# Kernel optimization log

Measured on AMD Instinct MI355X. Metric: run time of the kernel, lower is better.

The kernel has to match this reference:

```python
import jax, jax.numpy as jnp
import numpy as np


def setup_inputs() -> dict:
    key = jax.random.key(0)
    kq, kk, kv = jax.random.split(key, 3)
    shape = (2, 12, 4096, 64)  # [B, H, S, d]
    Q = jax.random.normal(kq, shape, dtype=jnp.float32)
    K = jax.random.normal(kk, shape, dtype=jnp.float32)
    V = jax.random.normal(kv, shape, dtype=jnp.float32)
    return {"Q": Q, "K": K, "V": V}


def reference(Q, K, V):
    d_k = K.shape[-1]
    scale = 1.0 / jnp.sqrt(jnp.asarray(d_k, dtype=Q.dtype))
    # [B,H,S,S] attention scores
    scores = jnp.einsum('bhqd,bhkd->bhqk', Q, K) * scale
    attn = jax.nn.softmax(scores, axis=-1)
    out = jnp.einsum('bhqk,bhkd->bhqd', attn, V)
    return out
```

## Files before the change

kernel.cpp:

```cpp
#include <hip/hip_runtime.h>


constexpr int Sseq = 4096;
constexpr int Dh   = 64;
constexpr int BM   = 128;
constexpr int BN   = 64;
constexpr int NT   = Sseq / BN;
constexpr float SHIFT = 10.0f;
constexpr float CINIT = -SHIFT + 0.002815047f;

typedef short bf16x8 __attribute__((ext_vector_type(8)));
typedef float f32x4  __attribute__((ext_vector_type(4)));

__device__ __forceinline__ unsigned short f2bf(float x) {
    union { float f; unsigned int u; } v; v.f = x;
    unsigned int r = v.u + 0x7fffu + ((v.u >> 16) & 1u);
    return (unsigned short)(r >> 16);
}

#if __has_builtin(__builtin_amdgcn_exp2f)
#define EXP2(x) __builtin_amdgcn_exp2f(x)
#else
#define EXP2(x) exp2f(x)
#endif

__device__ __forceinline__ int swz(int row, int blk8) {
    return row * 8 + (blk8 ^ (row & 7));
}

__device__ __forceinline__ void gld16(const void* g, void* l) {
    __builtin_amdgcn_global_load_lds(
        (const __attribute__((address_space(1))) void*)g,
        (__attribute__((address_space(3))) void*)l, 16, 0, 0);
}

union AFrag { unsigned int w[4]; bf16x8 b; };

__device__ __forceinline__ void s_phase(const unsigned short* __restrict__ sK,
                                        const bf16x8 (&qf)[2][2], f32x4 cinit,
                                        int lo, int quad, AFrag (&afW)[2][2]) {
    #pragma unroll
    for (int t = 0; t < 4; ++t) {
        const bf16x8 k0 = *reinterpret_cast<const bf16x8*>(&sK[swz(16 * t + lo, quad) * 8]);
        const bf16x8 k1 = *reinterpret_cast<const bf16x8*>(&sK[swz(16 * t + lo, 4 + quad) * 8]);
        #pragma unroll
        for (int u = 0; u < 2; ++u) {
            f32x4 s = __builtin_amdgcn_mfma_f32_16x16x32_bf16(k1, qf[u][1], cinit, 0, 0, 0);
            s = __builtin_amdgcn_mfma_f32_16x16x32_bf16(k0, qf[u][0], s, 0, 0, 0);
            union { float f; unsigned int v; } e0, e1, e2, e3;
            e0.f = EXP2(s[0]); e1.f = EXP2(s[1]);
            e2.f = EXP2(s[2]); e3.f = EXP2(s[3]);
            afW[u][t >> 1].w[2 * (t & 1) + 0] = __builtin_amdgcn_perm(e1.v, e0.v, 0x07060302u);
            afW[u][t >> 1].w[2 * (t & 1) + 1] = __builtin_amdgcn_perm(e3.v, e2.v, 0x07060302u);
        }
    }
}

__device__ __forceinline__ void pv_phase(const unsigned short* __restrict__ sVt,
                                         const AFrag (&afR)[2][2], bf16x8 onesb,
                                         int lo, int quad,
                                         f32x4 (&accv)[2][4], f32x4 (&acc5)[2]) {
    #pragma unroll
    for (int c = 0; c < 2; ++c) {
        #pragma unroll
        for (int u = 0; u < 2; ++u)
            acc5[u] = __builtin_amdgcn_mfma_f32_16x16x32_bf16(afR[u][c].b, onesb, acc5[u], 0, 0, 0);
        #pragma unroll
        for (int t2 = 0; t2 < 4; ++t2) {
            const bf16x8 vf = *reinterpret_cast<const bf16x8*>(&sVt[swz(16 * t2 + lo, 4 * c + quad) * 8]);
            #pragma unroll
            for (int u = 0; u < 2; ++u)
                accv[u][t2] = __builtin_amdgcn_mfma_f32_16x16x32_bf16(afR[u][c].b, vf, accv[u][t2], 0, 0, 0);
        }
    }
}

__global__ __launch_bounds__(256)
void preconv_kernel(const float* __restrict__ K, const float* __restrict__ V,
                    unsigned short* __restrict__ ws)
{
    __shared__ unsigned short tile[8192];
    unsigned short* tK = tile;
    unsigned short* tV = tile + 4096;

    const int kb = blockIdx.x, bh = blockIdx.y, tid = threadIdx.x;
    const float4* k4 = reinterpret_cast<const float4*>(K + ((size_t)bh * Sseq + kb * BN) * Dh);
    const float4* v4 = reinterpret_cast<const float4*>(V + ((size_t)bh * Sseq + kb * BN) * Dh);
    unsigned short* kimg = ws + (size_t)(bh * NT + kb) * 8192;

    float4 kv[4], vv[4];
    #pragma unroll
    for (int it = 0; it < 4; ++it) kv[it] = k4[it * 256 + tid];
    #pragma unroll
    for (int it = 0; it < 4; ++it) vv[it] = v4[it * 256 + tid];

    #pragma unroll
    for (int it = 0; it < 4; ++it) {
        const int f  = it * 256 + tid;
        const int r  = f >> 4;
        const int c4 = (f & 15) * 4;
        const int pr = (r & 32) | ((r & 4) << 2) | ((r & 24) >> 1) | (r & 3);
        unsigned int lo32 = (unsigned int)f2bf(kv[it].x) | ((unsigned int)f2bf(kv[it].y) << 16);
        unsigned int hi32 = (unsigned int)f2bf(kv[it].z) | ((unsigned int)f2bf(kv[it].w) << 16);
        *reinterpret_cast<uint2*>(&tK[swz(pr, c4 >> 3) * 8 + (c4 & 7)]) = make_uint2(lo32, hi32);
        tV[swz(c4 + 0, r >> 3) * 8 + (r & 7)] = f2bf(vv[it].x);
        tV[swz(c4 + 1, r >> 3) * 8 + (r & 7)] = f2bf(vv[it].y);
        tV[swz(c4 + 2, r >> 3) * 8 + (r & 7)] = f2bf(vv[it].z);
        tV[swz(c4 + 3, r >> 3) * 8 + (r & 7)] = f2bf(vv[it].w);
    }
    __syncthreads();

    const uint4* src = reinterpret_cast<const uint4*>(tile);
    uint4* dst = reinterpret_cast<uint4*>(kimg);
    #pragma unroll
    for (int i = 0; i < 4; ++i)
        dst[i * 256 + tid] = src[i * 256 + tid];
}

__global__ __launch_bounds__(256, 3)
void fattn_kernel(const float* __restrict__ Q, const unsigned short* __restrict__ ws,
                  float* __restrict__ O)
{
    __shared__ unsigned short sKV[3][8192];

    const int tid  = threadIdx.x;
    const int wave = tid >> 6;
    const int lane = tid & 63;
    const int lo   = lane & 15;
    const int quad = lane >> 4;

    const int qblk = blockIdx.x;
    const int bh   = blockIdx.y;

    const float* gQ = Q + (size_t)bh * Sseq * Dh;
    float*       gO = O + (size_t)bh * Sseq * Dh;

    const float qscale = 0.18033688011112042f;
    bf16x8 qf[2][2];
    #pragma unroll
    for (int u = 0; u < 2; ++u) {
        const int qrow = qblk * BM + wave * 32 + u * 16 + lo;
        const float* qp = gQ + (size_t)qrow * Dh + quad * 8;
        #pragma unroll
        for (int c = 0; c < 2; ++c) {
            float4 a = *reinterpret_cast<const float4*>(qp + c * 32);
            float4 b = *reinterpret_cast<const float4*>(qp + c * 32 + 4);
            qf[u][c][0] = (short)f2bf(a.x * qscale);
            qf[u][c][1] = (short)f2bf(a.y * qscale);
            qf[u][c][2] = (short)f2bf(a.z * qscale);
            qf[u][c][3] = (short)f2bf(a.w * qscale);
            qf[u][c][4] = (short)f2bf(b.x * qscale);
            qf[u][c][5] = (short)f2bf(b.y * qscale);
            qf[u][c][6] = (short)f2bf(b.z * qscale);
            qf[u][c][7] = (short)f2bf(b.w * qscale);
        }
    }

    bf16x8 onesb = (bf16x8)0;
    if (lo == 0) {
        #pragma unroll
        for (int j = 0; j < 8; ++j) onesb[j] = (short)0x3F80;
    }

    const f32x4 cinit = f32x4{CINIT, CINIT, CINIT, CINIT};

    f32x4 accv[2][4];
    f32x4 acc5[2];
    #pragma unroll
    for (int u = 0; u < 2; ++u) {
        acc5[u] = f32x4{0.f, 0.f, 0.f, 0.f};
        #pragma unroll
        for (int t = 0; t < 4; ++t) accv[u][t] = f32x4{0.f, 0.f, 0.f, 0.f};
    }

    AFrag afA[2][2], afB[2][2];

    const char* img = (const char*)(ws + (size_t)bh * NT * 8192);
    const int ubase = wave * 1024;
    const int goff  = ubase + lane * 16;

    auto dma = [&](int tile, int bufidx) {
        const char* nimg = img + (size_t)tile * 16384;
        char* dst = (char*)sKV[bufidx];
        gld16(nimg + goff,          dst + ubase);
        gld16(nimg + 4096  + goff,  dst + 4096  + ubase);
        gld16(nimg + 8192  + goff,  dst + 8192  + ubase);
        gld16(nimg + 12288 + goff,  dst + 12288 + ubase);
    };

    dma(0, 0);
    __syncthreads();
    dma(1, 1);
    s_phase(sKV[0], qf, cinit, lo, quad, afA);
    __syncthreads();
    dma(2, 2);

    int ibS = 1, ibP = 0;
    auto half = [&](int i, AFrag (&afW)[2][2], const AFrag (&afR)[2][2]) {
        const unsigned short* sK  = sKV[ibS];
        const unsigned short* sVt = sKV[ibP] + 4096;
        __builtin_amdgcn_s_setprio(1);
        s_phase(sK, qf, cinit, lo, quad, afW);
        pv_phase(sVt, afR, onesb, lo, quad, accv, acc5);
        __builtin_amdgcn_s_setprio(0);
        __syncthreads();
        if (i + 2 < NT) dma(i + 2, ibP);
        ibP = ibS;
        ibS = (ibS == 2) ? 0 : ibS + 1;
    };

    int i = 1;
    #pragma unroll 1
    for (int p = 0; p < 31; ++p) {
        half(i, afB, afA); ++i;
        half(i, afA, afB); ++i;
    }
    half(63, afB, afA);
    pv_phase(sKV[ibP] + 4096, afB, onesb, lo, quad, accv, acc5);

    #pragma unroll
    for (int u = 0; u < 2; ++u) {
        const int qbase = qblk * BM + wave * 32 + u * 16 + quad * 4;
        #pragma unroll
        for (int r = 0; r < 4; ++r) {
            const float ls  = __shfl(acc5[u][r], (lane & 48));
            const float inv = 1.0f / ls;
            float* op = gO + (size_t)(qbase + r) * Dh;
            #pragma unroll
            for (int t2 = 0; t2 < 4; ++t2)
                op[t2 * 16 + lo] = accv[u][t2][r] * inv;
        }
    }
}

constexpr int LD = 72;
__global__ __launch_bounds__(256, 2)
void fattn_fallback(const float* __restrict__ Q, const float* __restrict__ K,
                    const float* __restrict__ V, float* __restrict__ O)
{
    __shared__ unsigned short sK [BN * LD];
    __shared__ unsigned short sVt[Dh * LD];
    __shared__ unsigned short sP [4 * 16 * LD];

    const int tid  = threadIdx.x;
    const int wave = tid >> 6;
    const int lane = tid & 63;
    const int lo   = lane & 15;
    const int quad = lane >> 4;
    const int qblk = blockIdx.x;
    const int bh   = blockIdx.y;

    const float* gQ = Q + (size_t)bh * Sseq * Dh;
    const float* gK = K + (size_t)bh * Sseq * Dh;
    const float* gV = V + (size_t)bh * Sseq * Dh;
    float*       gO = O + (size_t)bh * Sseq * Dh;

    const float qscale = 0.18033688011112042f;
    bf16x8 qf[2];
    {
        const int qrow = qblk * 64 + wave * 16 + lo;
        const float* qp = gQ + (size_t)qrow * Dh + quad * 8;
        #pragma unroll
        for (int c = 0; c < 2; ++c) {
            float4 a = *reinterpret_cast<const float4*>(qp + c * 32);
            float4 b = *reinterpret_cast<const float4*>(qp + c * 32 + 4);
            qf[c][0] = (short)f2bf(a.x * qscale); qf[c][1] = (short)f2bf(a.y * qscale);
            qf[c][2] = (short)f2bf(a.z * qscale); qf[c][3] = (short)f2bf(a.w * qscale);
            qf[c][4] = (short)f2bf(b.x * qscale); qf[c][5] = (short)f2bf(b.y * qscale);
            qf[c][6] = (short)f2bf(b.z * qscale); qf[c][7] = (short)f2bf(b.w * qscale);
        }
    }

    float m_prev[4] = {-1e30f, -1e30f, -1e30f, -1e30f};
    float lsum[4]   = {0.f, 0.f, 0.f, 0.f};
    f32x4 accv[4];
    #pragma unroll
    for (int t = 0; t < 4; ++t) accv[t] = f32x4{0.f, 0.f, 0.f, 0.f};
    unsigned short* sPw = &sP[wave * 16 * LD];

    for (int kb = 0; kb < Sseq / BN; ++kb) {
        const float4* k4 = reinterpret_cast<const float4*>(gK + (size_t)kb * BN * Dh);
        const float4* v4 = reinterpret_cast<const float4*>(gV + (size_t)kb * BN * Dh);
        #pragma unroll
        for (int it = 0; it < 4; ++it) {
            const int f   = it * 256 + tid;
            const int row = f >> 4;
            const int c4  = (f & 15) * 4;
            float4 kv = k4[f];
            unsigned int lo32 = (unsigned int)f2bf(kv.x) | ((unsigned int)f2bf(kv.y) << 16);
            unsigned int hi32 = (unsigned int)f2bf(kv.z) | ((unsigned int)f2bf(kv.w) << 16);
            *reinterpret_cast<uint2*>(&sK[row * LD + c4]) = make_uint2(lo32, hi32);
            float4 vv = v4[f];
            sVt[(c4 + 0) * LD + row] = f2bf(vv.x);
            sVt[(c4 + 1) * LD + row] = f2bf(vv.y);
            sVt[(c4 + 2) * LD + row] = f2bf(vv.z);
            sVt[(c4 + 3) * LD + row] = f2bf(vv.w);
        }
        __syncthreads();

        float sc[4][4];
        #pragma unroll
        for (int t = 0; t < 4; ++t) {
            const bf16x8 k0 = *reinterpret_cast<const bf16x8*>(&sK[(t * 16 + lo) * LD + 0  + quad * 8]);
            const bf16x8 k1 = *reinterpret_cast<const bf16x8*>(&sK[(t * 16 + lo) * LD + 32 + quad * 8]);
            f32x4 s = f32x4{0.f, 0.f, 0.f, 0.f};
            s = __builtin_amdgcn_mfma_f32_16x16x32_bf16(qf[0], k0, s, 0, 0, 0);
            s = __builtin_amdgcn_mfma_f32_16x16x32_bf16(qf[1], k1, s, 0, 0, 0);
            sc[t][0] = s[0]; sc[t][1] = s[1]; sc[t][2] = s[2]; sc[t][3] = s[3];
        }

        float bm[4];
        #pragma unroll
        for (int r = 0; r < 4; ++r)
            bm[r] = fmaxf(fmaxf(sc[0][r], sc[1][r]), fmaxf(sc[2][r], sc[3][r]));
        #pragma unroll
        for (int m = 1; m <= 8; m <<= 1) {
            #pragma unroll
            for (int r = 0; r < 4; ++r) bm[r] = fmaxf(bm[r], __shfl_xor(bm[r], m));
        }
        float m_new[4], alpha[4];
        #pragma unroll
        for (int r = 0; r < 4; ++r) {
            m_new[r] = fmaxf(m_prev[r], bm[r]);
            alpha[r] = exp2f(m_prev[r] - m_new[r]);
            m_prev[r] = m_new[r];
        }
        float ps[4][4];
        float rs[4] = {0.f, 0.f, 0.f, 0.f};
        #pragma unroll
        for (int t = 0; t < 4; ++t) {
            #pragma unroll
            for (int r = 0; r < 4; ++r) { ps[t][r] = exp2f(sc[t][r] - m_new[r]); rs[r] += ps[t][r]; }
        }
        #pragma unroll
        for (int m = 1; m <= 8; m <<= 1) {
            #pragma unroll
            for (int r = 0; r < 4; ++r) rs[r] += __shfl_xor(rs[r], m);
        }
        #pragma unroll
        for (int r = 0; r < 4; ++r) lsum[r] = lsum[r] * alpha[r] + rs[r];
        #pragma unroll
        for (int t = 0; t < 4; ++t) {
            #pragma unroll
            for (int r = 0; r < 4; ++r) accv[t][r] *= alpha[r];
        }
        #pragma unroll
        for (int t = 0; t < 4; ++t) {
            #pragma unroll
            for (int r = 0; r < 4; ++r)
                sPw[(quad * 4 + r) * LD + t * 16 + lo] = f2bf(ps[t][r]);
        }
        #pragma unroll
        for (int c = 0; c < 2; ++c) {
            const bf16x8 af = *reinterpret_cast<const bf16x8*>(&sPw[lo * LD + c * 32 + quad * 8]);
            #pragma unroll
            for (int t2 = 0; t2 < 4; ++t2) {
                const bf16x8 vf = *reinterpret_cast<const bf16x8*>(&sVt[(t2 * 16 + lo) * LD + c * 32 + quad * 8]);
                accv[t2] = __builtin_amdgcn_mfma_f32_16x16x32_bf16(af, vf, accv[t2], 0, 0, 0);
            }
        }
        __syncthreads();
    }

    const int qbase = qblk * 64 + wave * 16 + quad * 4;
    #pragma unroll
    for (int r = 0; r < 4; ++r) {
        const float inv = 1.0f / lsum[r];
        float* op = gO + (size_t)(qbase + r) * Dh;
        #pragma unroll
        for (int t2 = 0; t2 < 4; ++t2)
            op[t2 * 16 + lo] = accv[t2][r] * inv;
    }
}

extern "C" void kernel_launch(void* const* d_in, const int* in_sizes, int n_in,
                              void* d_out, int out_size, void* d_ws, size_t ws_size,
                              hipStream_t stream) {
    const float* Q = (const float*)d_in[0];
    const float* K = (const float*)d_in[1];
    const float* V = (const float*)d_in[2];
    float* O = (float*)d_out;
    const int BH = in_sizes[0] / (Sseq * Dh);
    const size_t ws_needed = (size_t)BH * NT * 16384;
    if (ws_size >= ws_needed) {
        preconv_kernel<<<dim3(NT, BH), 256, 0, stream>>>(K, V, (unsigned short*)d_ws);
        fattn_kernel<<<dim3(Sseq / BM, BH), 256, 0, stream>>>(Q, (const unsigned short*)d_ws, O);
    } else {
        fattn_fallback<<<dim3(Sseq / 64, BH), 256, 0, stream>>>(Q, K, V, O);
    }
}
```

Measured before the change: 203.6 us.

## Load V fragments directly from global into registers, shrink LDS to double-buffered K

V tiles are no longer staged through LDS. Each wave now reads its pre-swizzled bf16 V fragments straight from the global workspace into registers at the start of each step, while only K keeps a two-slot LDS double buffer. This cuts LDS use from three 16KB buffers to two 8KB ones, which could raise occupancy, and removes the V LDS reads. In exchange, every wave issues redundant global loads for V with less latency hiding and more register pressure.

```diff
diff --git a/kernel.cpp b/kernel.cpp
--- a/kernel.cpp
+++ b/kernel.cpp
@@ -56,10 +56,19 @@
     }
 }
 
-__device__ __forceinline__ void pv_phase(const unsigned short* __restrict__ sVt,
-                                         const AFrag (&afR)[2][2], bf16x8 onesb,
-                                         int lo, int quad,
-                                         f32x4 (&accv)[2][4], f32x4 (&acc5)[2]) {
+__device__ __forceinline__ void pv_load(const char* __restrict__ vimg,
+                                        const unsigned int (&voff)[2][4],
+                                        bf16x8 (&vfr)[2][4]) {
+    #pragma unroll
+    for (int c = 0; c < 2; ++c)
+        #pragma unroll
+        for (int t2 = 0; t2 < 4; ++t2)
+            vfr[c][t2] = *reinterpret_cast<const bf16x8*>(vimg + voff[c][t2]);
+}
+
+__device__ __forceinline__ void pv_mfma(const bf16x8 (&vfr)[2][4],
+                                        const AFrag (&afR)[2][2], bf16x8 onesb,
+                                        f32x4 (&accv)[2][4], f32x4 (&acc5)[2]) {
     #pragma unroll
     for (int c = 0; c < 2; ++c) {
         #pragma unroll
@@ -67,10 +76,9 @@
             acc5[u] = __builtin_amdgcn_mfma_f32_16x16x32_bf16(afR[u][c].b, onesb, acc5[u], 0, 0, 0);
         #pragma unroll
         for (int t2 = 0; t2 < 4; ++t2) {
-            const bf16x8 vf = *reinterpret_cast<const bf16x8*>(&sVt[swz(16 * t2 + lo, 4 * c + quad) * 8]);
             #pragma unroll
             for (int u = 0; u < 2; ++u)
-                accv[u][t2] = __builtin_amdgcn_mfma_f32_16x16x32_bf16(afR[u][c].b, vf, accv[u][t2], 0, 0, 0);
+                accv[u][t2] = __builtin_amdgcn_mfma_f32_16x16x32_bf16(afR[u][c].b, vfr[c][t2], accv[u][t2], 0, 0, 0);
         }
     }
 }
@@ -121,7 +129,7 @@
 void fattn_kernel(const float* __restrict__ Q, const unsigned short* __restrict__ ws,
                   float* __restrict__ O)
 {
-    __shared__ unsigned short sKV[3][8192];
+    __shared__ unsigned short sKk[2][4096];
 
     const int tid  = threadIdx.x;
     const int wave = tid >> 6;
@@ -164,6 +172,13 @@
 
     const f32x4 cinit = f32x4{CINIT, CINIT, CINIT, CINIT};
 
+    unsigned int voff[2][4];
+    #pragma unroll
+    for (int c = 0; c < 2; ++c)
+        #pragma unroll
+        for (int t2 = 0; t2 < 4; ++t2)
+            voff[c][t2] = (unsigned int)(swz(16 * t2 + lo, 4 * c + quad) * 16);
+
     f32x4 accv[2][4];
     f32x4 acc5[2];
     #pragma unroll
@@ -179,34 +194,28 @@
     const int ubase = wave * 1024;
     const int goff  = ubase + lane * 16;
 
-    auto dma = [&](int tile, int bufidx) {
+    auto dmaK = [&](int tile, int bufidx) {
         const char* nimg = img + (size_t)tile * 16384;
-        char* dst = (char*)sKV[bufidx];
-        gld16(nimg + goff,          dst + ubase);
-        gld16(nimg + 4096  + goff,  dst + 4096  + ubase);
-        gld16(nimg + 8192  + goff,  dst + 8192  + ubase);
-        gld16(nimg + 12288 + goff,  dst + 12288 + ubase);
+        char* dst = (char*)sKk[bufidx];
+        gld16(nimg + goff,         dst + ubase);
+        gld16(nimg + 4096 + goff,  dst + 4096 + ubase);
     };
 
-    dma(0, 0);
+    dmaK(0, 0);
     __syncthreads();
-    dma(1, 1);
-    s_phase(sKV[0], qf, cinit, lo, quad, afA);
+    dmaK(1, 1);
+    s_phase(sKk[0], qf, cinit, lo, quad, afA);
     __syncthreads();
-    dma(2, 2);
-
-    int ibS = 1, ibP = 0;
+
     auto half = [&](int i, AFrag (&afW)[2][2], const AFrag (&afR)[2][2]) {
-        const unsigned short* sK  = sKV[ibS];
-        const unsigned short* sVt = sKV[ibP] + 4096;
+        bf16x8 vfr[2][4];
+        pv_load(img + (size_t)(i - 1) * 16384 + 8192, voff, vfr);
+        if (i + 1 < NT) dmaK(i + 1, (i + 1) & 1);
         __builtin_amdgcn_s_setprio(1);
-        s_phase(sK, qf, cinit, lo, quad, afW);
-        pv_phase(sVt, afR, onesb, lo, quad, accv, acc5);
+        s_phase(sKk[i & 1], qf, cinit, lo, quad, afW);
+        pv_mfma(vfr, afR, onesb, accv, acc5);
         __builtin_amdgcn_s_setprio(0);
         __syncthreads();
-        if (i + 2 < NT) dma(i + 2, ibP);
-        ibP = ibS;
-        ibS = (ibS == 2) ? 0 : ibS + 1;
     };
 
     int i = 1;
@@ -216,7 +225,11 @@
         half(i, afA, afB); ++i;
     }
     half(63, afB, afA);
-    pv_phase(sKV[ibP] + 4096, afB, onesb, lo, quad, accv, acc5);
+    {
+        bf16x8 vfr[2][4];
+        pv_load(img + (size_t)63 * 16384 + 8192, voff, vfr);
+        pv_mfma(vfr, afB, onesb, accv, acc5);
+    }
 
     #pragma unroll
     for (int u = 0; u < 2; ++u) {
```

Result: slower. 277.0 us (+36.1%).
